# Kernel optimization log

Measured on AMD Instinct MI355X. Metric: run time of the kernel, lower is better.

## Reference

```python
import jax, jax.numpy as jnp
import numpy as np

NC, K, SD = 8, 1024, 64
L = NC * SD
B = 8192
TAU = 0.07
COMMIT_W = 1.0
CONTRAST_W = 1.0
EPS = 1e-12


def setup_inputs() -> dict:
    key = jax.random.key(0)
    kz, ke = jax.random.split(key)
    z = jax.random.normal(kz, (B, L), dtype=jnp.float32)
    embeddings = jax.random.normal(ke, (NC, K, SD), dtype=jnp.float32)
    return {"z": z, "embeddings": embeddings}


def reference(z, embeddings):
    sg = jax.lax.stop_gradient
    Bn, Ln = z.shape
    nc, k, sd = embeddings.shape
    zr = z.reshape(Bn, nc, sd)  # (B, nc, sd)

    # squared distances via ||z||^2 - 2 z.e + ||e||^2 -> (B, nc, K), avoids (B,nc,K,sd)
    z2 = jnp.sum(zr * zr, axis=-1)[:, :, None]
    e2 = jnp.sum(embeddings * embeddings, axis=-1)[None, :, :]
    cross = jnp.einsum('bnd,nkd->bnk', zr, embeddings)
    dists = z2 - 2.0 * cross + e2
    indices = jnp.argmin(dists, axis=-1)  # (B, nc)

    # codebook gather
    quant_splits = embeddings[jnp.arange(nc)[None, :], indices]  # (B, nc, sd)
    quant_z = quant_splits.reshape(Bn, Ln)

    commit_loss = jnp.mean((sg(quant_z) - z) ** 2)
    embed_loss = jnp.mean((quant_z - sg(z)) ** 2)
    total_commit = commit_loss + embed_loss

    quant_z_st = z + sg(quant_z - z)

    z_norm = z / jnp.maximum(jnp.linalg.norm(z, axis=-1, keepdims=True), EPS)
    q_det = sg(quant_z)
    q_norm = q_det / jnp.maximum(jnp.linalg.norm(q_det, axis=-1, keepdims=True), EPS)
    logits = jnp.matmul(q_norm, z_norm.T) / TAU  # (B, B)
    # cross-entropy with labels = arange(B)
    contrastive = jnp.mean(jax.nn.logsumexp(logits, axis=1) - jnp.diagonal(logits))

    return (quant_z_st, COMMIT_W * total_commit, CONTRAST_W * contrastive, indices)
```

## Files before the change

### kernel.cpp

```cpp
#include <hip/hip_runtime.h>
#include <cstdint>
#include <cstddef>

#define NCB   8
#define KC    1024
#define SDIM  64
#define LDIM  512
#define BATCH 8192
#define INV_TAU (1.0f/0.07f)
#define K2E  20.60992915555662f
#define STR8 272

typedef __bf16 bf16_t;
typedef bf16_t bf16x8 __attribute__((ext_vector_type(8)));
typedef float  floatx4 __attribute__((ext_vector_type(4)));
typedef int    intx8  __attribute__((ext_vector_type(8)));

__device__ __forceinline__ unsigned short f2bf(float f) {
    union { float f; unsigned int u; } c; c.f = f;
    unsigned int u = c.u;
    u += 0x7fffu + ((u >> 16) & 1u);
    return (unsigned short)(u >> 16);
}
__device__ __forceinline__ float bf2f(unsigned short h) {
    union { unsigned int u; float f; } c; c.u = ((unsigned int)h) << 16;
    return c.f;
}
__device__ __forceinline__ float exp2_fast(float x) {
    float r; asm("v_exp_f32 %0, %1" : "=v"(r) : "v"(x)); return r;
}

__device__ __forceinline__ void merge2(float& m1, int& i1, float& m2, int& i2,
                                       float o1, int j1, float o2, int j2) {
    bool a = o1 < m1;
    float f1 = a ? o1 : m1; int g1 = a ? j1 : i1;
    float f2 = a ? m1 : o1; int g2 = a ? i1 : j1;
    bool b = o2 < m2;
    float f3 = b ? o2 : m2; int g3 = b ? j2 : i2;
    bool c = f3 < f2;
    m1 = f1; i1 = g1;
    m2 = c ? f3 : f2; i2 = c ? g3 : g2;
}

__global__ __launch_bounds__(256) void
k_pre(const float* __restrict__ z, const float* __restrict__ emb,
      float* __restrict__ e2, unsigned short* __restrict__ eh,
      unsigned short* __restrict__ el, unsigned short* __restrict__ zh,
      unsigned short* __restrict__ zl, float* __restrict__ accs) {
    int bid = blockIdx.x;
    if (bid < 4096) {
        int id = bid * 256 + threadIdx.x;
        float4 v = ((const float4*)z)[id];
        ushort4 h, l;
        h.x=f2bf(v.x); l.x=f2bf(v.x-bf2f(h.x));
        h.y=f2bf(v.y); l.y=f2bf(v.y-bf2f(h.y));
        h.z=f2bf(v.z); l.z=f2bf(v.z-bf2f(h.z));
        h.w=f2bf(v.w); l.w=f2bf(v.w-bf2f(h.w));
        ((ushort4*)zh)[id]=h; ((ushort4*)zl)[id]=l;
    } else {
        int id = (bid - 4096) * 256 + threadIdx.x;
        const float4* e4 = (const float4*)(emb + (size_t)id * SDIM);
        ushort4* eh4 = (ushort4*)(eh + (size_t)id * SDIM);
        ushort4* el4 = (ushort4*)(el + (size_t)id * SDIM);
        float s0=0.f,s1=0.f,s2=0.f,s3=0.f;
#pragma unroll
        for (int i=0;i<16;i++){ float4 v=e4[i];
            s0=fmaf(v.x,v.x,s0); s1=fmaf(v.y,v.y,s1);
            s2=fmaf(v.z,v.z,s2); s3=fmaf(v.w,v.w,s3);
            ushort4 h, l;
            h.x=f2bf(v.x); l.x=f2bf(v.x-bf2f(h.x));
            h.y=f2bf(v.y); l.y=f2bf(v.y-bf2f(h.y));
            h.z=f2bf(v.z); l.z=f2bf(v.z-bf2f(h.z));
            h.w=f2bf(v.w); l.w=f2bf(v.w-bf2f(h.w));
            eh4[i]=h; el4[i]=l;
        }
        e2[id] = (s0+s1)+(s2+s3);
        if (id==0){ accs[0]=0.f; accs[1]=0.f; accs[2]=0.f; }
    }
}

__device__ __forceinline__ double dist64d(const float* __restrict__ e,
                                          const float* __restrict__ zg) {
    double se=0.0, sz=0.0;
#pragma unroll 8
    for (int i=0;i<64;i++){ double ev=(double)e[i];
        se = fma(ev,ev,se); sz = fma(ev,(double)zg[i],sz); }
    return se - 2.0*sz;
}

__global__ __launch_bounds__(256,2) void
k_argmin(const unsigned short* __restrict__ zh, const unsigned short* __restrict__ zl,
         const unsigned short* __restrict__ eh, const unsigned short* __restrict__ el,
         const float* __restrict__ e2, const float* __restrict__ z,
         const float* __restrict__ emb, float* __restrict__ out_q,
         float* __restrict__ out_idx, float* __restrict__ accs) {
    __shared__ unsigned short Ah[128*72], Al[128*72];
    __shared__ unsigned short Bh[128*72], Bl[128*72];
    __shared__ float e2s[128];
    __shared__ float mM[2][128][2];
    __shared__ int   mI[2][128][2];

    const int tid = threadIdx.x;
    const int n   = blockIdx.y;
    const int i0  = blockIdx.x * 128;
    const int wid = tid >> 6, lane = tid & 63;
    const int wm = wid & 1, wn = wid >> 1;
    const int c  = lane & 15, qq = lane >> 4;

#pragma unroll
    for (int s=0;s<4;s++){
        int seg = tid + s*256; int r = seg>>3, sg = seg&7;
        size_t go = (size_t)(i0+r)*LDIM + n*SDIM + sg*8;
        *(uint4*)(&Ah[r*72+sg*8]) = *(const uint4*)(zh + go);
        *(uint4*)(&Al[r*72+sg*8]) = *(const uint4*)(zl + go);
    }

    float m1[16], m2[16]; int i1v[16], i2v[16];
#pragma unroll
    for (int j=0;j<16;j++){ m1[j]=3.4e38f; m2[j]=3.4e38f; i1v[j]=0; i2v[j]=0; }

    const unsigned short* ehn = eh + (size_t)n*KC*SDIM;
    const unsigned short* eln = el + (size_t)n*KC*SDIM;
    const float* e2n = e2 + n*KC;

    for (int jt=0; jt<8; jt++){
        const int j0 = jt*128;
        __syncthreads();
#pragma unroll
        for (int s=0;s<4;s++){
            int seg = tid + s*256; int r = seg>>3, sg = seg&7;
            size_t go = (size_t)(j0+r)*SDIM + sg*8;
            *(uint4*)(&Bh[r*72+sg*8]) = *(const uint4*)(ehn + go);
            *(uint4*)(&Bl[r*72+sg*8]) = *(const uint4*)(eln + go);
        }
        if (tid < 128) e2s[tid] = e2n[j0+tid];
        __syncthreads();

        floatx4 acc[4][4];
#pragma unroll
        for (int mt=0;mt<4;mt++)
#pragma unroll
            for (int nt=0;nt<4;nt++) acc[mt][nt] = (floatx4){0.f,0.f,0.f,0.f};

#pragma unroll
        for (int t=0;t<2;t++){
            bf16x8 ah[4], al[4], bh[4], bl[4];
#pragma unroll
            for (int mt=0;mt<4;mt++){
                ah[mt] = *(const bf16x8*)(&Ah[(wm*64+mt*16+c)*72 + t*32 + qq*8]);
                al[mt] = *(const bf16x8*)(&Al[(wm*64+mt*16+c)*72 + t*32 + qq*8]);
            }
#pragma unroll
            for (int nt=0;nt<4;nt++){
                bh[nt] = *(const bf16x8*)(&Bh[(wn*64+nt*16+c)*72 + t*32 + qq*8]);
                bl[nt] = *(const bf16x8*)(&Bl[(wn*64+nt*16+c)*72 + t*32 + qq*8]);
            }
#pragma unroll
            for (int mt=0;mt<4;mt++)
#pragma unroll
                for (int nt=0;nt<4;nt++){
                    acc[mt][nt] = __builtin_amdgcn_mfma_f32_16x16x32_bf16(ah[mt], bh[nt], acc[mt][nt], 0,0,0);
                    acc[mt][nt] = __builtin_amdgcn_mfma_f32_16x16x32_bf16(ah[mt], bl[nt], acc[mt][nt], 0,0,0);
                    acc[mt][nt] = __builtin_amdgcn_mfma_f32_16x16x32_bf16(al[mt], bh[nt], acc[mt][nt], 0,0,0);
                }
        }

#pragma unroll
        for (int nt=0;nt<4;nt++){
            const int colb = wn*64 + nt*16 + c;
            float e2v = e2s[colb];
            int kidx = j0 + colb;
#pragma unroll
            for (int mt=0;mt<4;mt++)
#pragma unroll
                for (int reg=0;reg<4;reg++){
                    float d = fmaf(-2.0f, acc[mt][nt][reg], e2v);
                    int s = mt*4+reg;
                    float om1 = m1[s]; int oi1 = i1v[s];
                    bool lt1 = d < om1;
                    bool lt2 = d < m2[s];
                    m2[s]  = lt1 ? om1 : (lt2 ? d : m2[s]);
                    i2v[s] = lt1 ? oi1 : (lt2 ? kidx : i2v[s]);
                    m1[s]  = lt1 ? d : om1;
                    i1v[s] = lt1 ? kidx : oi1;
                }
        }
    }

#pragma unroll
    for (int off=1; off<16; off<<=1){
#pragma unroll
        for (int s=0;s<16;s++){
            float o1 = __shfl_xor(m1[s], off);
            float o2 = __shfl_xor(m2[s], off);
            int   j1 = __shfl_xor(i1v[s], off);
            int   j2 = __shfl_xor(i2v[s], off);
            merge2(m1[s], i1v[s], m2[s], i2v[s], o1, j1, o2, j2);
        }
    }
    if (c == 0){
#pragma unroll
        for (int s=0;s<16;s++){
            int row = wm*64 + (s>>2)*16 + qq*4 + (s&3);
            mM[wn][row][0] = m1[s]; mM[wn][row][1] = m2[s];
            mI[wn][row][0] = i1v[s]; mI[wn][row][1] = i2v[s];
        }
    }
    __syncthreads();

    if (tid < 128){
        int b = i0 + tid;
        float b1 = mM[0][tid][0], b2v = mM[0][tid][1];
        int  ii1 = mI[0][tid][0], ii2 = mI[0][tid][1];
        merge2(b1, ii1, b2v, ii2, mM[1][tid][0], mI[1][tid][0],
                                  mM[1][tid][1], mI[1][tid][1]);

        const float* eb = emb + (size_t)n*KC*SDIM;
        const float* zg = z + (size_t)b*LDIM + n*SDIM;
        if (b2v - b1 < 2e-2f) {
            double d1 = dist64d(eb + (size_t)ii1*SDIM, zg);
            double d2 = dist64d(eb + (size_t)ii2*SDIM, zg);
            if (d2 < d1 || (d2 == d1 && ii2 < ii1)) ii1 = ii2;
        }

        const float4* q4 = (const float4*)(eb + (size_t)ii1*SDIM);
        const float4* z4 = (const float4*)zg;
        float4* oq = (float4*)(out_q + (size_t)b*LDIM + n*SDIM);
        float cs = 0.f;
#pragma unroll
        for (int i=0;i<16;i++){
            float4 v = q4[i]; float4 zv = z4[i];
            oq[i] = v;
            float d0=v.x-zv.x, d1=v.y-zv.y, d2=v.z-zv.z, d3=v.w-zv.w;
            cs += d0*d0 + d1*d1 + d2*d2 + d3*d3;
        }
        out_idx[b*NCB + n] = (float)ii1;

        for (int off=32; off; off>>=1) cs += __shfl_down(cs, off);
        if ((tid & 63)==0) atomicAdd(&accs[0], cs);
    }
}

__global__ __launch_bounds__(256) void
k_norm(const float* __restrict__ z, const float* __restrict__ q,
       unsigned char* __restrict__ zn8, unsigned char* __restrict__ qn8,
       float* __restrict__ diag) {
    const int b = blockIdx.x, tid = threadIdx.x;
    const size_t base = (size_t)b*LDIM;
    float2 zv = ((const float2*)(z+base))[tid];
    float2 qv = ((const float2*)(q+base))[tid];
    float sz = zv.x*zv.x + zv.y*zv.y;
    float sq = qv.x*qv.x + qv.y*qv.y;
    float sqz= qv.x*zv.x + qv.y*zv.y;
    for (int off=32; off; off>>=1){
        sz+=__shfl_down(sz,off); sq+=__shfl_down(sq,off); sqz+=__shfl_down(sqz,off);
    }
    __shared__ float red[3][4];
    __shared__ float bc[2];
    int w = tid>>6;
    if ((tid&63)==0){ red[0][w]=sz; red[1][w]=sq; red[2][w]=sqz; }
    __syncthreads();
    if (tid==0){
        float tz = red[0][0]+red[0][1]+red[0][2]+red[0][3];
        float tq = red[1][0]+red[1][1]+red[1][2]+red[1][3];
        float tz_q = red[2][0]+red[2][1]+red[2][2]+red[2][3];
        float inz = 1.0f/fmaxf(sqrtf(tz), 1e-12f);
        float inq = 1.0f/fmaxf(sqrtf(tq), 1e-12f);
        bc[0]=inz; bc[1]=inq;
        diag[b] = tz_q*inz*inq*INV_TAU;
    }
    __syncthreads();
    float inz=bc[0], inq=bc[1];
    int pz = __builtin_amdgcn_cvt_pk_fp8_f32(zv.x*inz, zv.y*inz, 0, false);
    int pq = __builtin_amdgcn_cvt_pk_fp8_f32(qv.x*inq, qv.y*inq, 0, false);
    ((unsigned short*)(zn8+base))[tid] = (unsigned short)(pz & 0xffff);
    ((unsigned short*)(qn8+base))[tid] = (unsigned short)(pq & 0xffff);
}

__global__ __launch_bounds__(256,2) void
k_logits(const unsigned char* __restrict__ qn8, const unsigned char* __restrict__ zn8,
         float* __restrict__ Spart) {
    __shared__ unsigned char As[128*STR8];
    __shared__ unsigned char Bs[128*STR8];
    const int tid  = threadIdx.x;
    const int i0   = blockIdx.x * 128;
    const int chnk = blockIdx.y;
    const int wid  = tid >> 6, lane = tid & 63;
    const int wm = wid & 1, wn = wid >> 1;
    const int c  = lane & 15, qq = lane >> 4;

    float S[16];
#pragma unroll
    for (int i=0;i<16;i++) S[i] = 0.f;

    for (int jt=0;jt<8;jt++){
        const int j0 = chnk*1024 + jt*128;
        floatx4 acc[4][4];
#pragma unroll
        for (int mt=0;mt<4;mt++)
#pragma unroll
            for (int nt=0;nt<4;nt++) acc[mt][nt] = (floatx4){0.f,0.f,0.f,0.f};

        for (int kk=0;kk<512;kk+=256){
            __syncthreads();
#pragma unroll
            for (int s=0;s<8;s++){
                int seg = tid + s*256;
                int r = seg >> 4, sg = seg & 15;
                *(uint4*)(&As[r*STR8 + sg*16]) =
                    *(const uint4*)(qn8 + (size_t)(i0+r)*LDIM + kk + sg*16);
            }
#pragma unroll
            for (int s=0;s<8;s++){
                int seg = tid + s*256;
                int r = seg >> 4, sg = seg & 15;
                *(uint4*)(&Bs[r*STR8 + sg*16]) =
                    *(const uint4*)(zn8 + (size_t)(j0+r)*LDIM + kk + sg*16);
            }
            __syncthreads();
#pragma unroll
            for (int t=0;t<2;t++){
                intx8 af[4], bfr[4];
#pragma unroll
                for (int mt=0;mt<4;mt++){
                    const unsigned char* p = &As[(wm*64+mt*16+c)*STR8 + t*128 + qq*32];
                    union { intx8 v; uint4 h[2]; } u;
                    u.h[0] = *(const uint4*)(p);
                    u.h[1] = *(const uint4*)(p+16);
                    af[mt] = u.v;
                }
#pragma unroll
                for (int nt=0;nt<4;nt++){
                    const unsigned char* p = &Bs[(wn*64+nt*16+c)*STR8 + t*128 + qq*32];
                    union { intx8 v; uint4 h[2]; } u;
                    u.h[0] = *(const uint4*)(p);
                    u.h[1] = *(const uint4*)(p+16);
                    bfr[nt] = u.v;
                }
#pragma unroll
                for (int mt=0;mt<4;mt++)
#pragma unroll
                    for (int nt=0;nt<4;nt++)
                        acc[mt][nt] = __builtin_amdgcn_mfma_scale_f32_16x16x128_f8f6f4(
                            af[mt], bfr[nt], acc[mt][nt],
                            0, 0,
                            0, 127,
                            0, 127);
            }
        }

#pragma unroll
        for (int mt=0;mt<4;mt++)
#pragma unroll
            for (int reg=0;reg<4;reg++){
                float e0 = exp2_fast(fmaf(acc[mt][0][reg], K2E, -K2E));
                float e1 = exp2_fast(fmaf(acc[mt][1][reg], K2E, -K2E));
                float e2v= exp2_fast(fmaf(acc[mt][2][reg], K2E, -K2E));
                float e3 = exp2_fast(fmaf(acc[mt][3][reg], K2E, -K2E));
                S[mt*4+reg] += (e0+e1)+(e2v+e3);
            }
    }

#pragma unroll
    for (int off=1; off<16; off<<=1)
#pragma unroll
        for (int s=0;s<16;s++) S[s] += __shfl_xor(S[s], off);

    if (c == 0){
        const int p = chnk*2 + wn;
#pragma unroll
        for (int mt=0;mt<4;mt++)
#pragma unroll
            for (int reg=0;reg<4;reg++){
                int row = i0 + wm*64 + mt*16 + qq*4 + reg;
                Spart[p*BATCH + row] = S[mt*4+reg];
            }
    }
}

__global__ __launch_bounds__(256) void
k_finalize(const float* __restrict__ Spart, const float* __restrict__ diag,
           float* __restrict__ accs, float* __restrict__ out_s) {
    int r = blockIdx.x*256 + threadIdx.x;
    float Ssum = 0.f;
#pragma unroll
    for (int p=0;p<16;p++) Ssum += Spart[p*BATCH + r];
    float val = INV_TAU + logf(Ssum) - diag[r];
    for (int off=32; off; off>>=1) val += __shfl_down(val, off);
    if ((threadIdx.x & 63)==0) atomicAdd(&accs[1], val);
    __syncthreads();
    if (threadIdx.x == 0){
        __threadfence();
        unsigned int old = __float_as_uint(atomicAdd(&accs[2], 1.0f));
        if (old == __float_as_uint(31.0f)) {
            __threadfence();
            float a0 = atomicAdd(&accs[0], 0.0f);
            float a1 = atomicAdd(&accs[1], 0.0f);
            out_s[0] = 2.0f*a0 / (float)((size_t)BATCH*LDIM);
            out_s[1] = a1 / (float)BATCH;
        }
    }
}

extern "C" void kernel_launch(void* const* d_in, const int* in_sizes, int n_in,
                              void* d_out, int out_size, void* d_ws, size_t ws_size,
                              hipStream_t stream) {
    const float* z   = (const float*)d_in[0];
    const float* emb = (const float*)d_in[1];
    float* out = (float*)d_out;
    float* out_q       = out;
    float* out_scalars = out + 4194304;
    float* out_idx     = out + 4194306;

    float* wsf   = (float*)d_ws;
    float* e2    = wsf;
    float* accs  = wsf + 8192;
    float* diag  = wsf + 8704;
    float* Spart = wsf + 16896;
    unsigned short* zh = (unsigned short*)(Spart + 32*BATCH);
    unsigned short* zl = zh + (size_t)BATCH*LDIM;
    unsigned short* eh = zl + (size_t)BATCH*LDIM;
    unsigned short* el = eh + (size_t)NCB*KC*SDIM;
    unsigned char* qn8 = (unsigned char*)zh;
    unsigned char* zn8 = qn8 + (size_t)BATCH*LDIM;

    k_pre    <<<4128,        256, 0, stream>>>(z, emb, e2, eh, el, zh, zl, accs);
    k_argmin <<<dim3(64,8),  256, 0, stream>>>(zh, zl, eh, el, e2, z, emb,
                                               out_q, out_idx, accs);
    k_norm   <<<BATCH,       256, 0, stream>>>(z, out_q, zn8, qn8, diag);
    k_logits <<<dim3(64,8),  256, 0, stream>>>(qn8, zn8, Spart);
    k_finalize<<<32,         256, 0, stream>>>(Spart, diag, accs, out_scalars);
}
```

Measured before the change: 188.8 us.

## Shrink codebook tile and LDS footprint to fit three blocks per CU

The argmin kernel now stages 64 codebook entries per iteration instead of 128, running twice as many iterations. It changes the LDS row stride from 72 to 68 and reuses the B tile buffer for the final min/index merge scratch, which needs an extra barrier. Launch bounds rise to three blocks per CU. The aim is higher occupancy to hide latency, in exchange for more barriers and smaller per-iteration MFMA work, plus possible register pressure or bank-conflict changes from the new stride.

```diff
diff --git a/kernel.cpp b/kernel.cpp
--- a/kernel.cpp
+++ b/kernel.cpp
@@ -10,6 +10,7 @@
 #define INV_TAU (1.0f/0.07f)
 #define K2E  20.60992915555662f
 #define STR8 272
+#define ASTR 68
 
 typedef __bf16 bf16_t;
 typedef bf16_t bf16x8 __attribute__((ext_vector_type(8)));
@@ -88,17 +89,17 @@
     return se - 2.0*sz;
 }
 
-__global__ __launch_bounds__(256,2) void
+__global__ __launch_bounds__(256,3) void
 k_argmin(const unsigned short* __restrict__ zh, const unsigned short* __restrict__ zl,
          const unsigned short* __restrict__ eh, const unsigned short* __restrict__ el,
          const float* __restrict__ e2, const float* __restrict__ z,
          const float* __restrict__ emb, float* __restrict__ out_q,
          float* __restrict__ out_idx, float* __restrict__ accs) {
-    __shared__ unsigned short Ah[128*72], Al[128*72];
-    __shared__ unsigned short Bh[128*72], Bl[128*72];
-    __shared__ float e2s[128];
-    __shared__ float mM[2][128][2];
-    __shared__ int   mI[2][128][2];
+    __shared__ unsigned short Ah[128*ASTR], Al[128*ASTR];
+    __shared__ unsigned short Bh[64*ASTR],  Bl[64*ASTR];
+    __shared__ float e2s[64];
+    float* mMf = (float*)Bh;
+    int*   mIf = ((int*)Bh) + 512;
 
     const int tid = threadIdx.x;
     const int n   = blockIdx.y;
@@ -111,8 +112,8 @@
     for (int s=0;s<4;s++){
         int seg = tid + s*256; int r = seg>>3, sg = seg&7;
         size_t go = (size_t)(i0+r)*LDIM + n*SDIM + sg*8;
-        *(uint4*)(&Ah[r*72+sg*8]) = *(const uint4*)(zh + go);
-        *(uint4*)(&Al[r*72+sg*8]) = *(const uint4*)(zl + go);
+        *(uint4*)(&Ah[r*ASTR+sg*8]) = *(const uint4*)(zh + go);
+        *(uint4*)(&Al[r*ASTR+sg*8]) = *(const uint4*)(zl + go);
     }
 
     float m1[16], m2[16]; int i1v[16], i2v[16];
@@ -123,42 +124,42 @@
     const unsigned short* eln = el + (size_t)n*KC*SDIM;
     const float* e2n = e2 + n*KC;
 
-    for (int jt=0; jt<8; jt++){
-        const int j0 = jt*128;
+    for (int jt=0; jt<16; jt++){
+        const int j0 = jt*64;
         __syncthreads();
 #pragma unroll
-        for (int s=0;s<4;s++){
+        for (int s=0;s<2;s++){
             int seg = tid + s*256; int r = seg>>3, sg = seg&7;
             size_t go = (size_t)(j0+r)*SDIM + sg*8;
-            *(uint4*)(&Bh[r*72+sg*8]) = *(const uint4*)(ehn + go);
-            *(uint4*)(&Bl[r*72+sg*8]) = *(const uint4*)(eln + go);
-        }
-        if (tid < 128) e2s[tid] = e2n[j0+tid];
+            *(uint4*)(&Bh[r*ASTR+sg*8]) = *(const uint4*)(ehn + go);
+            *(uint4*)(&Bl[r*ASTR+sg*8]) = *(const uint4*)(eln + go);
+        }
+        if (tid < 64) e2s[tid] = e2n[j0+tid];
         __syncthreads();
 
-        floatx4 acc[4][4];
+        floatx4 acc[4][2];
 #pragma unroll
         for (int mt=0;mt<4;mt++)
 #pragma unroll
-            for (int nt=0;nt<4;nt++) acc[mt][nt] = (floatx4){0.f,0.f,0.f,0.f};
+            for (int nt=0;nt<2;nt++) acc[mt][nt] = (floatx4){0.f,0.f,0.f,0.f};
 
 #pragma unroll
         for (int t=0;t<2;t++){
-            bf16x8 ah[4], al[4], bh[4], bl[4];
+            bf16x8 ah[4], al[4], bh[2], bl[2];
 #pragma unroll
             for (int mt=0;mt<4;mt++){
-                ah[mt] = *(const bf16x8*)(&Ah[(wm*64+mt*16+c)*72 + t*32 + qq*8]);
-                al[mt] = *(const bf16x8*)(&Al[(wm*64+mt*16+c)*72 + t*32 + qq*8]);
-            }
-#pragma unroll
-            for (int nt=0;nt<4;nt++){
-                bh[nt] = *(const bf16x8*)(&Bh[(wn*64+nt*16+c)*72 + t*32 + qq*8]);
-                bl[nt] = *(const bf16x8*)(&Bl[(wn*64+nt*16+c)*72 + t*32 + qq*8]);
+                ah[mt] = *(const bf16x8*)(&Ah[(wm*64+mt*16+c)*ASTR + t*32 + qq*8]);
+                al[mt] = *(const bf16x8*)(&Al[(wm*64+mt*16+c)*ASTR + t*32 + qq*8]);
+            }
+#pragma unroll
+            for (int nt=0;nt<2;nt++){
+                bh[nt] = *(const bf16x8*)(&Bh[(wn*32+nt*16+c)*ASTR + t*32 + qq*8]);
+                bl[nt] = *(const bf16x8*)(&Bl[(wn*32+nt*16+c)*ASTR + t*32 + qq*8]);
             }
 #pragma unroll
             for (int mt=0;mt<4;mt++)
 #pragma unroll
-                for (int nt=0;nt<4;nt++){
+                for (int nt=0;nt<2;nt++){
                     acc[mt][nt] = __builtin_amdgcn_mfma_f32_16x16x32_bf16(ah[mt], bh[nt], acc[mt][nt], 0,0,0);
                     acc[mt][nt] = __builtin_amdgcn_mfma_f32_16x16x32_bf16(ah[mt], bl[nt], acc[mt][nt], 0,0,0);
                     acc[mt][nt] = __builtin_amdgcn_mfma_f32_16x16x32_bf16(al[mt], bh[nt], acc[mt][nt], 0,0,0);
@@ -166,8 +167,8 @@
         }
 
 #pragma unroll
-        for (int nt=0;nt<4;nt++){
-            const int colb = wn*64 + nt*16 + c;
+        for (int nt=0;nt<2;nt++){
+            const int colb = wn*32 + nt*16 + c;
             float e2v = e2s[colb];
             int kidx = j0 + colb;
 #pragma unroll
@@ -198,22 +199,23 @@
             merge2(m1[s], i1v[s], m2[s], i2v[s], o1, j1, o2, j2);
         }
     }
+    __syncthreads();
     if (c == 0){
 #pragma unroll
         for (int s=0;s<16;s++){
             int row = wm*64 + (s>>2)*16 + qq*4 + (s&3);
-            mM[wn][row][0] = m1[s]; mM[wn][row][1] = m2[s];
-            mI[wn][row][0] = i1v[s]; mI[wn][row][1] = i2v[s];
+            mMf[wn*256 + row*2 + 0] = m1[s]; mMf[wn*256 + row*2 + 1] = m2[s];
+            mIf[wn*256 + row*2 + 0] = i1v[s]; mIf[wn*256 + row*2 + 1] = i2v[s];
         }
     }
     __syncthreads();
 
     if (tid < 128){
         int b = i0 + tid;
-        float b1 = mM[0][tid][0], b2v = mM[0][tid][1];
-        int  ii1 = mI[0][tid][0], ii2 = mI[0][tid][1];
-        merge2(b1, ii1, b2v, ii2, mM[1][tid][0], mI[1][tid][0],
-                                  mM[1][tid][1], mI[1][tid][1]);
+        float b1 = mMf[tid*2+0], b2v = mMf[tid*2+1];
+        int  ii1 = mIf[tid*2+0], ii2 = mIf[tid*2+1];
+        merge2(b1, ii1, b2v, ii2, mMf[256+tid*2+0], mIf[256+tid*2+0],
+                                  mMf[256+tid*2+1], mIf[256+tid*2+1]);
 
         const float* eb = emb + (size_t)n*KC*SDIM;
         const float* zg = z + (size_t)b*LDIM + n*SDIM;
```

New measurement: 211.9 us. 12.2% more time.

## Fuse z bf16 split into argmin kernel and pack top-2 distance/index keys

Applied to the files above, without the earlier changes.

Moves the hi/lo bf16 split of z from the preprocessing kernel into the argmin kernel's tile load, so zh/zl no longer go through global memory and k_pre shrinks to the codebook-only part. The per-thread top-2 tracking now packs a biased, truncated float distance and a 10-bit index into one unsigned key, so updates and shuffle merges use integer min/max instead of compare-and-select chains. Truncating the mantissa coarsens distance resolution, which the wider double-precision recheck threshold (0.08) is meant to compensate for. The DBIAS offset keeps distances positive so unsigned ordering matches float ordering.

```diff
diff --git a/kernel.cpp b/kernel.cpp
--- a/kernel.cpp
+++ b/kernel.cpp
@@ -10,6 +10,7 @@
 #define INV_TAU (1.0f/0.07f)
 #define K2E  20.60992915555662f
 #define STR8 272
+#define DBIAS 256.0f
 
 typedef __bf16 bf16_t;
 typedef bf16_t bf16x8 __attribute__((ext_vector_type(8)));
@@ -30,53 +31,28 @@
     float r; asm("v_exp_f32 %0, %1" : "=v"(r) : "v"(x)); return r;
 }
 
-__device__ __forceinline__ void merge2(float& m1, int& i1, float& m2, int& i2,
-                                       float o1, int j1, float o2, int j2) {
-    bool a = o1 < m1;
-    float f1 = a ? o1 : m1; int g1 = a ? j1 : i1;
-    float f2 = a ? m1 : o1; int g2 = a ? i1 : j1;
-    bool b = o2 < m2;
-    float f3 = b ? o2 : m2; int g3 = b ? j2 : i2;
-    bool c = f3 < f2;
-    m1 = f1; i1 = g1;
-    m2 = c ? f3 : f2; i2 = c ? g3 : g2;
-}
-
 __global__ __launch_bounds__(256) void
-k_pre(const float* __restrict__ z, const float* __restrict__ emb,
-      float* __restrict__ e2, unsigned short* __restrict__ eh,
-      unsigned short* __restrict__ el, unsigned short* __restrict__ zh,
-      unsigned short* __restrict__ zl, float* __restrict__ accs) {
-    int bid = blockIdx.x;
-    if (bid < 4096) {
-        int id = bid * 256 + threadIdx.x;
-        float4 v = ((const float4*)z)[id];
+k_pre(const float* __restrict__ emb, float* __restrict__ e2,
+      unsigned short* __restrict__ eh, unsigned short* __restrict__ el,
+      float* __restrict__ accs) {
+    int id = blockIdx.x * 256 + threadIdx.x;
+    const float4* e4 = (const float4*)(emb + (size_t)id * SDIM);
+    ushort4* eh4 = (ushort4*)(eh + (size_t)id * SDIM);
+    ushort4* el4 = (ushort4*)(el + (size_t)id * SDIM);
+    float s0=0.f,s1=0.f,s2=0.f,s3=0.f;
+#pragma unroll
+    for (int i=0;i<16;i++){ float4 v=e4[i];
+        s0=fmaf(v.x,v.x,s0); s1=fmaf(v.y,v.y,s1);
+        s2=fmaf(v.z,v.z,s2); s3=fmaf(v.w,v.w,s3);
         ushort4 h, l;
         h.x=f2bf(v.x); l.x=f2bf(v.x-bf2f(h.x));
         h.y=f2bf(v.y); l.y=f2bf(v.y-bf2f(h.y));
         h.z=f2bf(v.z); l.z=f2bf(v.z-bf2f(h.z));
         h.w=f2bf(v.w); l.w=f2bf(v.w-bf2f(h.w));
-        ((ushort4*)zh)[id]=h; ((ushort4*)zl)[id]=l;
-    } else {
-        int id = (bid - 4096) * 256 + threadIdx.x;
-        const float4* e4 = (const float4*)(emb + (size_t)id * SDIM);
-        ushort4* eh4 = (ushort4*)(eh + (size_t)id * SDIM);
-        ushort4* el4 = (ushort4*)(el + (size_t)id * SDIM);
-        float s0=0.f,s1=0.f,s2=0.f,s3=0.f;
-#pragma unroll
-        for (int i=0;i<16;i++){ float4 v=e4[i];
-            s0=fmaf(v.x,v.x,s0); s1=fmaf(v.y,v.y,s1);
-            s2=fmaf(v.z,v.z,s2); s3=fmaf(v.w,v.w,s3);
-            ushort4 h, l;
-            h.x=f2bf(v.x); l.x=f2bf(v.x-bf2f(h.x));
-            h.y=f2bf(v.y); l.y=f2bf(v.y-bf2f(h.y));
-            h.z=f2bf(v.z); l.z=f2bf(v.z-bf2f(h.z));
-            h.w=f2bf(v.w); l.w=f2bf(v.w-bf2f(h.w));
-            eh4[i]=h; el4[i]=l;
-        }
-        e2[id] = (s0+s1)+(s2+s3);
-        if (id==0){ accs[0]=0.f; accs[1]=0.f; accs[2]=0.f; }
-    }
+        eh4[i]=h; el4[i]=l;
+    }
+    e2[id] = (s0+s1)+(s2+s3);
+    if (id==0){ accs[0]=0.f; accs[1]=0.f; accs[2]=0.f; }
 }
 
 __device__ __forceinline__ double dist64d(const float* __restrict__ e,
@@ -89,16 +65,14 @@
 }
 
 __global__ __launch_bounds__(256,2) void
-k_argmin(const unsigned short* __restrict__ zh, const unsigned short* __restrict__ zl,
-         const unsigned short* __restrict__ eh, const unsigned short* __restrict__ el,
+k_argmin(const unsigned short* __restrict__ eh, const unsigned short* __restrict__ el,
          const float* __restrict__ e2, const float* __restrict__ z,
          const float* __restrict__ emb, float* __restrict__ out_q,
          float* __restrict__ out_idx, float* __restrict__ accs) {
     __shared__ unsigned short Ah[128*72], Al[128*72];
     __shared__ unsigned short Bh[128*72], Bl[128*72];
     __shared__ float e2s[128];
-    __shared__ float mM[2][128][2];
-    __shared__ int   mI[2][128][2];
+    __shared__ unsigned int mK[2][128][2];
 
     const int tid = threadIdx.x;
     const int n   = blockIdx.y;
@@ -108,16 +82,22 @@
     const int c  = lane & 15, qq = lane >> 4;
 
 #pragma unroll
-    for (int s=0;s<4;s++){
-        int seg = tid + s*256; int r = seg>>3, sg = seg&7;
-        size_t go = (size_t)(i0+r)*LDIM + n*SDIM + sg*8;
-        *(uint4*)(&Ah[r*72+sg*8]) = *(const uint4*)(zh + go);
-        *(uint4*)(&Al[r*72+sg*8]) = *(const uint4*)(zl + go);
-    }
-
-    float m1[16], m2[16]; int i1v[16], i2v[16];
-#pragma unroll
-    for (int j=0;j<16;j++){ m1[j]=3.4e38f; m2[j]=3.4e38f; i1v[j]=0; i2v[j]=0; }
+    for (int s=0;s<8;s++){
+        int seg = tid + s*256;
+        int r = seg >> 4, sg = seg & 15;
+        float4 v = *(const float4*)(z + (size_t)(i0+r)*LDIM + n*SDIM + sg*4);
+        ushort4 h, l;
+        h.x=f2bf(v.x); l.x=f2bf(v.x-bf2f(h.x));
+        h.y=f2bf(v.y); l.y=f2bf(v.y-bf2f(h.y));
+        h.z=f2bf(v.z); l.z=f2bf(v.z-bf2f(h.z));
+        h.w=f2bf(v.w); l.w=f2bf(v.w-bf2f(h.w));
+        *(ushort4*)(&Ah[r*72+sg*4]) = h;
+        *(ushort4*)(&Al[r*72+sg*4]) = l;
+    }
+
+    unsigned int k1[16], k2[16];
+#pragma unroll
+    for (int j=0;j<16;j++){ k1[j]=0xFFFFFFFFu; k2[j]=0xFFFFFFFFu; }
 
     const unsigned short* ehn = eh + (size_t)n*KC*SDIM;
     const unsigned short* eln = el + (size_t)n*KC*SDIM;
@@ -133,7 +113,7 @@
             *(uint4*)(&Bh[r*72+sg*8]) = *(const uint4*)(ehn + go);
             *(uint4*)(&Bl[r*72+sg*8]) = *(const uint4*)(eln + go);
         }
-        if (tid < 128) e2s[tid] = e2n[j0+tid];
+        if (tid < 128) e2s[tid] = e2n[j0+tid] + DBIAS;
         __syncthreads();
 
         floatx4 acc[4][4];
@@ -169,20 +149,17 @@
         for (int nt=0;nt<4;nt++){
             const int colb = wn*64 + nt*16 + c;
             float e2v = e2s[colb];
-            int kidx = j0 + colb;
+            unsigned int kidx = (unsigned int)(j0 + colb);
 #pragma unroll
             for (int mt=0;mt<4;mt++)
 #pragma unroll
                 for (int reg=0;reg<4;reg++){
                     float d = fmaf(-2.0f, acc[mt][nt][reg], e2v);
+                    unsigned int key = (__float_as_uint(d) & 0xFFFFFC00u) | kidx;
                     int s = mt*4+reg;
-                    float om1 = m1[s]; int oi1 = i1v[s];
-                    bool lt1 = d < om1;
-                    bool lt2 = d < m2[s];
-                    m2[s]  = lt1 ? om1 : (lt2 ? d : m2[s]);
-                    i2v[s] = lt1 ? oi1 : (lt2 ? kidx : i2v[s]);
-                    m1[s]  = lt1 ? d : om1;
-                    i1v[s] = lt1 ? kidx : oi1;
+                    unsigned int o1 = k1[s];
+                    k2[s] = min(k2[s], max(key, o1));
+                    k1[s] = min(o1, key);
                 }
         }
     }
@@ -191,33 +168,36 @@
     for (int off=1; off<16; off<<=1){
 #pragma unroll
         for (int s=0;s<16;s++){
-            float o1 = __shfl_xor(m1[s], off);
-            float o2 = __shfl_xor(m2[s], off);
-            int   j1 = __shfl_xor(i1v[s], off);
-            int   j2 = __shfl_xor(i2v[s], off);
-            merge2(m1[s], i1v[s], m2[s], i2v[s], o1, j1, o2, j2);
+            unsigned int o1 = __shfl_xor(k1[s], off);
+            unsigned int o2 = __shfl_xor(k2[s], off);
+            unsigned int n1 = min(k1[s], o1);
+            k2[s] = min( max(k1[s], o1), min(k2[s], o2) );
+            k1[s] = n1;
         }
     }
     if (c == 0){
 #pragma unroll
         for (int s=0;s<16;s++){
             int row = wm*64 + (s>>2)*16 + qq*4 + (s&3);
-            mM[wn][row][0] = m1[s]; mM[wn][row][1] = m2[s];
-            mI[wn][row][0] = i1v[s]; mI[wn][row][1] = i2v[s];
+            mK[wn][row][0] = k1[s]; mK[wn][row][1] = k2[s];
         }
     }
     __syncthreads();
 
     if (tid < 128){
         int b = i0 + tid;
-        float b1 = mM[0][tid][0], b2v = mM[0][tid][1];
-        int  ii1 = mI[0][tid][0], ii2 = mI[0][tid][1];
-        merge2(b1, ii1, b2v, ii2, mM[1][tid][0], mI[1][tid][0],
-                                  mM[1][tid][1], mI[1][tid][1]);
+        unsigned int a1 = mK[0][tid][0], a2 = mK[0][tid][1];
+        unsigned int c1 = mK[1][tid][0], c2 = mK[1][tid][1];
+        unsigned int f1 = min(a1, c1);
+        unsigned int f2 = min( max(a1, c1), min(a2, c2) );
+        int ii1 = (int)(f1 & 0x3FFu);
+        int ii2 = (int)(f2 & 0x3FFu);
+        float d1q = __uint_as_float(f1 & 0xFFFFFC00u);
+        float d2q = __uint_as_float(f2 & 0xFFFFFC00u);
 
         const float* eb = emb + (size_t)n*KC*SDIM;
         const float* zg = z + (size_t)b*LDIM + n*SDIM;
-        if (b2v - b1 < 2e-2f) {
+        if (d2q - d1q < 0.08f) {
             double d1 = dist64d(eb + (size_t)ii1*SDIM, zg);
             double d2 = dist64d(eb + (size_t)ii2*SDIM, zg);
             if (d2 < d1 || (d2 == d1 && ii2 < ii1)) ii1 = ii2;
@@ -417,15 +397,13 @@
     float* accs  = wsf + 8192;
     float* diag  = wsf + 8704;
     float* Spart = wsf + 16896;
-    unsigned short* zh = (unsigned short*)(Spart + 32*BATCH);
-    unsigned short* zl = zh + (size_t)BATCH*LDIM;
-    unsigned short* eh = zl + (size_t)BATCH*LDIM;
+    unsigned char* qn8 = (unsigned char*)(Spart + 32*BATCH);
+    unsigned char* zn8 = qn8 + (size_t)BATCH*LDIM;
+    unsigned short* eh = (unsigned short*)(zn8 + (size_t)BATCH*LDIM);
     unsigned short* el = eh + (size_t)NCB*KC*SDIM;
-    unsigned char* qn8 = (unsigned char*)zh;
-    unsigned char* zn8 = qn8 + (size_t)BATCH*LDIM;
-
-    k_pre    <<<4128,        256, 0, stream>>>(z, emb, e2, eh, el, zh, zl, accs);
-    k_argmin <<<dim3(64,8),  256, 0, stream>>>(zh, zl, eh, el, e2, z, emb,
+
+    k_pre    <<<32,          256, 0, stream>>>(emb, e2, eh, el, accs);
+    k_argmin <<<dim3(64,8),  256, 0, stream>>>(eh, el, e2, z, emb,
                                                out_q, out_idx, accs);
     k_norm   <<<BATCH,       256, 0, stream>>>(z, out_q, zn8, qn8, diag);
     k_logits <<<dim3(64,8),  256, 0, stream>>>(qn8, zn8, Spart);
```

After: 173.3 us. -8.2%, faster.
